# Optimization experiments

Hardware: AMD Instinct MI355X
Metric: run time of the kernel (lower is better)

Reference implementation:

```python
import jax, jax.numpy as jnp
import numpy as np

H = 512  # hidden_size

def setup_inputs() -> dict:
    key = jax.random.key(0)
    ks = jax.random.split(key, 5)
    B, S = 2, 512
    feats = jax.random.normal(ks[0], (B, S, H), dtype=jnp.float32)
    # torch Linear init ~ U(-1/sqrt(in), 1/sqrt(in)); scaled normals are fine for a reference
    W1 = jax.random.normal(ks[1], (2 * H, H), dtype=jnp.float32) / np.sqrt(2 * H)
    b1 = jnp.zeros((H,), dtype=jnp.float32)
    W2 = jax.random.normal(ks[2], (H, H // 2), dtype=jnp.float32) / np.sqrt(H)
    b2 = jnp.zeros((H // 2,), dtype=jnp.float32)
    W3 = jax.random.normal(ks[3], (H // 2, 1), dtype=jnp.float32) / np.sqrt(H // 2)
    b3 = jnp.zeros((1,), dtype=jnp.float32)
    return {"features": feats, "W1": W1, "b1": b1, "W2": W2, "b2": b2, "W3": W3, "b3": b3}


def reference(features, W1, b1, W2, b2, W3, b3):
    # cat([f_i, f_j]) @ W1 == f_i @ W1[:H] + f_j @ W1[H:]
    # Precompute the two halves once per residue instead of per pair.
    a = jnp.einsum('bsh,hk->bsk', features, W1[:H])          # [B,S,H]
    c = jnp.einsum('bsh,hk->bsk', features, W1[H:])          # [B,S,H]
    h1 = jax.nn.relu(a[:, :, None, :] + c[:, None, :, :] + b1)  # [B,S,S,H]
    # Dropout(0.1) is identity at inference.
    h2 = jax.nn.relu(jnp.einsum('bijh,hk->bijk', h1, W2) + b2)  # [B,S,S,H//2]
    logits = jnp.einsum('bijk,ko->bijo', h2, W3) + b3            # [B,S,S,1]
    return jax.nn.sigmoid(logits[..., 0])                        # [B,S,S]
```

## Files before the change

### kernel.cpp

```cpp
#include <hip/hip_runtime.h>

#define S_DIM 512
#define H_DIM 512
#define NH 256
#define TI 8
#define TJ 8

#define AS1 __attribute__((address_space(1)))
#define AS3 __attribute__((address_space(3)))

typedef _Float16 half8 __attribute__((ext_vector_type(8)));
typedef _Float16 half4 __attribute__((ext_vector_type(4)));
typedef float f32x4 __attribute__((ext_vector_type(4)));

__device__ __forceinline__ int swz(int r) { return ((r & 1) << 2) | (r >> 1); }

__global__ __launch_bounds__(256) void convert_all_kernel(const float* __restrict__ feats,
        const float* __restrict__ W1, const float* __restrict__ W2,
        _Float16* __restrict__ f16, _Float16* __restrict__ w1L, _Float16* __restrict__ w2L) {
    int blk = blockIdx.x;
    if (blk < 512) {
        int t = blk * 256 + threadIdx.x;
        float4 v = ((const float4*)feats)[t];
        half4 h;
        h.x = (_Float16)v.x; h.y = (_Float16)v.y; h.z = (_Float16)v.z; h.w = (_Float16)v.w;
        ((half4*)f16)[t] = h;
    } else if (blk < 768) {
        int t = (blk - 512) * 256 + threadIdx.x;
        int gcb = t >> 10, n = t & 1023;
        const float* src = (n < H_DIM) ? &W1[(size_t)(gcb * 8) * H_DIM + n]
                                       : &W1[(size_t)(H_DIM + gcb * 8) * H_DIM + (n - H_DIM)];
        half8 v;
#pragma unroll
        for (int j = 0; j < 8; j++) v[j] = (_Float16)src[(size_t)j * H_DIM];
        *(half8*)&w1L[((size_t)gcb * 1024 + n) * 8] = v;
    } else {
        int t = (blk - 768) * 256 + threadIdx.x;
        int gcb = t >> 8, n = t & 255;
        half8 v;
#pragma unroll
        for (int j = 0; j < 8; j++) v[j] = (_Float16)W2[(size_t)(gcb * 8 + j) * NH + n];
        *(half8*)&w2L[((size_t)gcb * 256 + n) * 8] = v;
    }
}

__global__ __launch_bounds__(256) void prep_mfma_kernel(const _Float16* __restrict__ f16,
        const _Float16* __restrict__ w1L, const float* __restrict__ b1,
        _Float16* __restrict__ aH, _Float16* __restrict__ cH) {
    const int n0 = blockIdx.x * 64, m0 = blockIdx.y * 64;
    const int tid = threadIdx.x, wave = tid >> 6, lane = tid & 63;
    const int quad = lane >> 4, l16 = lane & 15;
    const int wm = wave >> 1, wn = wave & 1;
    int mrow[2], ncol[2];
#pragma unroll
    for (int mt = 0; mt < 2; mt++) mrow[mt] = m0 + wm * 32 + mt * 16 + l16;
#pragma unroll
    for (int nt = 0; nt < 2; nt++) ncol[nt] = n0 + wn * 32 + nt * 16 + l16;
    f32x4 acc[2][2];
#pragma unroll
    for (int mt = 0; mt < 2; mt++)
#pragma unroll
        for (int nt = 0; nt < 2; nt++) acc[mt][nt] = (f32x4)0.f;
#pragma unroll
    for (int ks = 0; ks < 16; ks++) {
        int gcb = ks * 4 + quad;
        half8 af[2], bf[2];
#pragma unroll
        for (int mt = 0; mt < 2; mt++)
            af[mt] = *(const half8*)&f16[(size_t)mrow[mt] * H_DIM + gcb * 8];
#pragma unroll
        for (int nt = 0; nt < 2; nt++)
            bf[nt] = *(const half8*)&w1L[((size_t)gcb * 1024 + ncol[nt]) * 8];
#pragma unroll
        for (int nt = 0; nt < 2; nt++)
#pragma unroll
            for (int mt = 0; mt < 2; mt++)
                acc[mt][nt] = __builtin_amdgcn_mfma_f32_16x16x32_f16(af[mt], bf[nt],
                                                                     acc[mt][nt], 0, 0, 0);
    }
    const bool first_half = (n0 < H_DIM);
#pragma unroll
    for (int nt = 0; nt < 2; nt++) {
        float bias = first_half ? b1[ncol[nt]] : 0.f;
#pragma unroll
        for (int mt = 0; mt < 2; mt++)
#pragma unroll
            for (int r = 0; r < 4; r++) {
                int m = m0 + wm * 32 + mt * 16 + quad * 4 + r;
                float v = acc[mt][nt][r] + bias;
                if (first_half) aH[(size_t)m * H_DIM + ncol[nt]] = (_Float16)v;
                else            cH[(size_t)m * H_DIM + (ncol[nt] - H_DIM)] = (_Float16)v;
            }
    }
}

__global__ __launch_bounds__(256, 4) void pair_kernel(
        const _Float16* __restrict__ aH, const _Float16* __restrict__ cH,
        const _Float16* __restrict__ w2L,
        const float* __restrict__ b2, const float* __restrict__ W3,
        const float* __restrict__ b3, float* __restrict__ out) {
    const int jt = blockIdx.x, it = blockIdx.y, b = blockIdx.z;
    const int i0 = it * TI, j0 = jt * TJ;

    __shared__ __align__(16) _Float16 sa[TI * H_DIM];
    __shared__ __align__(16) _Float16 sc[TJ * H_DIM];
    __shared__ __align__(16) _Float16 afb[2][4][512];
    __shared__ float spart[4][64];

    const int tid = threadIdx.x;
    const int wave = tid >> 6, lane = tid & 63;
    const int quad = lane >> 4, l16 = lane & 15;
    const int nb = wave * 64;

#pragma unroll
    for (int rr0 = 0; rr0 < 2; rr0++) {
        int rr = rr0 * 4 + wave;
        int gc = lane ^ swz(rr & 7);
        __builtin_amdgcn_global_load_lds(
            (const AS1 unsigned int*)&aH[((size_t)(b * S_DIM + i0 + rr)) * H_DIM + gc * 8],
            (AS3 unsigned int*)&sa[rr * H_DIM], 16, 0, 0);
        __builtin_amdgcn_global_load_lds(
            (const AS1 unsigned int*)&cH[((size_t)(b * S_DIM + j0 + rr)) * H_DIM + gc * 8],
            (AS3 unsigned int*)&sc[rr * H_DIM], 16, 0, 0);
    }

    const int hl = l16 >> 3;
    const int ilW = wave * 2 + hl;
    const int saoffW = ilW * H_DIM;
    const int swzAW = swz(ilW);
    const int jl = l16 & 7;
    const int scoff = jl * H_DIM, swzC = swz(jl);

    f32x4 acc[4][4];
#pragma unroll
    for (int mt = 0; mt < 4; mt++)
#pragma unroll
        for (int nt = 0; nt < 4; nt++) acc[mt][nt] = (f32x4)0.f;

    const _Float16* bp = &w2L[((size_t)quad * 256 + nb + l16) * 8];

    half8 bnxt[4];
#pragma unroll
    for (int nt = 0; nt < 4; nt++) bnxt[nt] = *(const half8*)&bp[nt * 16 * 8];

    __syncthreads();

    {
        const int gcb = quad;
        half8 va = *(const half8*)&sa[saoffW + ((gcb ^ swzAW) * 8)];
        half8 vc = *(const half8*)&sc[scoff + ((gcb ^ swzC) * 8)];
        half8 af = __builtin_elementwise_max(va + vc, (half8)(_Float16)0.f);
        *(half8*)&afb[0][wave][lane * 8] = af;
    }
    asm volatile("s_waitcnt lgkmcnt(0)" ::: "memory");
    __builtin_amdgcn_s_barrier();
    __builtin_amdgcn_sched_barrier(0);

#pragma unroll
    for (int ks = 0; ks < 16; ks++) {
        const int buf = ks & 1;
        half8 bf[4];
#pragma unroll
        for (int nt = 0; nt < 4; nt++) bf[nt] = bnxt[nt];
        if (ks < 15) {
            const _Float16* bn = bp + (size_t)4 * 256 * 8;
#pragma unroll
            for (int nt = 0; nt < 4; nt++) bnxt[nt] = *(const half8*)&bn[nt * 16 * 8];
            bp = bn;
            const int gcb = (ks + 1) * 4 + quad;
            half8 va = *(const half8*)&sa[saoffW + ((gcb ^ swzAW) * 8)];
            half8 vc = *(const half8*)&sc[scoff + ((gcb ^ swzC) * 8)];
            half8 af = __builtin_elementwise_max(va + vc, (half8)(_Float16)0.f);
            *(half8*)&afb[buf ^ 1][wave][lane * 8] = af;
        }
        half8 afr[4];
#pragma unroll
        for (int mt = 0; mt < 4; mt++)
            afr[mt] = *(const half8*)&afb[buf][mt][lane * 8];
#pragma unroll
        for (int nt = 0; nt < 4; nt++)
#pragma unroll
            for (int mt = 0; mt < 4; mt++)
                acc[mt][nt] = __builtin_amdgcn_mfma_f32_16x16x32_f16(afr[mt], bf[nt],
                                                                     acc[mt][nt], 0, 0, 0);
        if (ks < 15) {
            asm volatile("s_waitcnt lgkmcnt(0)" ::: "memory");
            __builtin_amdgcn_s_barrier();
            __builtin_amdgcn_sched_barrier(0);
        }
    }

    float b2v[4], w3v[4];
#pragma unroll
    for (int nt = 0; nt < 4; nt++) {
        int n = nb + nt * 16 + l16;
        b2v[nt] = b2[n];
        w3v[nt] = W3[n];
    }
    float ps[4][4];
#pragma unroll
    for (int mt = 0; mt < 4; mt++)
#pragma unroll
        for (int r = 0; r < 4; r++) {
            float s = 0.f;
#pragma unroll
            for (int nt = 0; nt < 4; nt++) {
                float v = acc[mt][nt][r] + b2v[nt];
                v = v > 0.f ? v : 0.f;
                s += v * w3v[nt];
            }
            ps[mt][r] = s;
        }
#pragma unroll
    for (int mt = 0; mt < 4; mt++)
#pragma unroll
        for (int r = 0; r < 4; r++) {
            float s = ps[mt][r];
            s += __shfl_xor(s, 8, 16);
            s += __shfl_xor(s, 4, 16);
            s += __shfl_xor(s, 2, 16);
            s += __shfl_xor(s, 1, 16);
            ps[mt][r] = s;
        }
    if (l16 == 0) {
#pragma unroll
        for (int mt = 0; mt < 4; mt++)
#pragma unroll
            for (int r = 0; r < 4; r++)
                spart[wave][mt * 16 + quad * 4 + r] = ps[mt][r];
    }
    __syncthreads();
    if (tid < 64) {
        float tot = spart[0][tid] + spart[1][tid] + spart[2][tid] + spart[3][tid] + b3[0];
        float sg = 1.f / (1.f + __expf(-tot));
        int i = i0 + (tid >> 3), j = j0 + (tid & 7);
        out[(size_t)b * S_DIM * S_DIM + (size_t)i * S_DIM + j] = sg;
    }
}

extern "C" void kernel_launch(void* const* d_in, const int* in_sizes, int n_in,
                              void* d_out, int out_size, void* d_ws, size_t ws_size,
                              hipStream_t stream) {
    const float* feats = (const float*)d_in[0];
    const float* W1 = (const float*)d_in[1];
    const float* b1 = (const float*)d_in[2];
    const float* W2 = (const float*)d_in[3];
    const float* b2 = (const float*)d_in[4];
    const float* W3 = (const float*)d_in[5];
    const float* b3 = (const float*)d_in[6];
    float* out = (float*)d_out;

    const int B = in_sizes[0] / (S_DIM * H_DIM);
    const int M = B * S_DIM;

    char* ws = (char*)d_ws;
    _Float16* f16  = (_Float16*)ws;
    _Float16* aH   = (_Float16*)(ws + (1 << 20));
    _Float16* cH   = (_Float16*)(ws + (2 << 20));
    _Float16* w1L  = (_Float16*)(ws + (3 << 20));
    _Float16* w2L  = (_Float16*)(ws + (4 << 20));

    convert_all_kernel<<<832, 256, 0, stream>>>(feats, W1, W2, f16, w1L, w2L);
    prep_mfma_kernel<<<dim3(16, M / 64), 256, 0, stream>>>(f16, w1L, b1, aH, cH);
    pair_kernel<<<dim3(S_DIM / TJ, S_DIM / TI, B), 256, 0, stream>>>(aH, cH, w2L, b2, W3, b3, out);
}
```

Before: 201.2 us.

## Switch pair GEMM from 16x16x32 to 32x32x16 MFMA tiles

Replaces the 16x16x32 f16 MFMA tiling (4x4 accumulators per wave) with 32x32x16 MFMAs (2x2 f32x16 accumulators). This changes how the relu(a+c) fragments and the W2 fragments are distributed across lanes and waves, and rewrites the epilogue reduction to match the 32-lane output layout. It also raises wave priority around the MFMA block with s_setprio. The aim is fewer MFMA issues and better operand reuse per instruction, at the cost of a more intricate lane and row mapping that has to stay consistent with the precomputed weight layout.

```diff
diff --git a/kernel.cpp b/kernel.cpp
--- a/kernel.cpp
+++ b/kernel.cpp
@@ -12,6 +12,7 @@
 typedef _Float16 half8 __attribute__((ext_vector_type(8)));
 typedef _Float16 half4 __attribute__((ext_vector_type(4)));
 typedef float f32x4 __attribute__((ext_vector_type(4)));
+typedef float f32x16 __attribute__((ext_vector_type(16)));
 
 __device__ __forceinline__ int swz(int r) { return ((r & 1) << 2) | (r >> 1); }
 
@@ -109,7 +110,7 @@
 
     const int tid = threadIdx.x;
     const int wave = tid >> 6, lane = tid & 63;
-    const int quad = lane >> 4, l16 = lane & 15;
+    const int l32 = lane & 31, hi = lane >> 5;
     const int nb = wave * 64;
 
 #pragma unroll
@@ -124,31 +125,32 @@
             (AS3 unsigned int*)&sc[rr * H_DIM], 16, 0, 0);
     }
 
-    const int hl = l16 >> 3;
-    const int ilW = wave * 2 + hl;
+    const int kstW = wave >> 1, mtW = wave & 1;
+    const int ilW = mtW * 4 + (l32 >> 3);
     const int saoffW = ilW * H_DIM;
     const int swzAW = swz(ilW);
-    const int jl = l16 & 7;
+    const int jl = l32 & 7;
     const int scoff = jl * H_DIM, swzC = swz(jl);
 
-    f32x4 acc[4][4];
-#pragma unroll
-    for (int mt = 0; mt < 4; mt++)
-#pragma unroll
-        for (int nt = 0; nt < 4; nt++) acc[mt][nt] = (f32x4)0.f;
-
-    const _Float16* bp = &w2L[((size_t)quad * 256 + nb + l16) * 8];
+    f32x16 acc[2][2];
+#pragma unroll
+    for (int mt = 0; mt < 2; mt++)
+#pragma unroll
+        for (int nt = 0; nt < 2; nt++) acc[mt][nt] = (f32x16)0.f;
+
+    const _Float16* bp = &w2L[((size_t)(hi * 256 + nb + l32)) * 8];
 
     half8 bnxt[4];
 #pragma unroll
-    for (int nt = 0; nt < 4; nt++) bnxt[nt] = *(const half8*)&bp[nt * 16 * 8];
+    for (int q = 0; q < 4; q++)
+        bnxt[q] = *(const half8*)&bp[(q >> 1) * 4096 + (q & 1) * 256];
 
     __syncthreads();
 
     {
-        const int gcb = quad;
-        half8 va = *(const half8*)&sa[saoffW + ((gcb ^ swzAW) * 8)];
-        half8 vc = *(const half8*)&sc[scoff + ((gcb ^ swzC) * 8)];
+        const int chunk = kstW * 2 + hi;
+        half8 va = *(const half8*)&sa[saoffW + ((chunk ^ swzAW) * 8)];
+        half8 vc = *(const half8*)&sc[scoff + ((chunk ^ swzC) * 8)];
         half8 af = __builtin_elementwise_max(va + vc, (half8)(_Float16)0.f);
         *(half8*)&afb[0][wave][lane * 8] = af;
     }
@@ -161,28 +163,33 @@
         const int buf = ks & 1;
         half8 bf[4];
 #pragma unroll
-        for (int nt = 0; nt < 4; nt++) bf[nt] = bnxt[nt];
+        for (int q = 0; q < 4; q++) bf[q] = bnxt[q];
         if (ks < 15) {
-            const _Float16* bn = bp + (size_t)4 * 256 * 8;
-#pragma unroll
-            for (int nt = 0; nt < 4; nt++) bnxt[nt] = *(const half8*)&bn[nt * 16 * 8];
+            const _Float16* bn = bp + (size_t)8192;
+#pragma unroll
+            for (int q = 0; q < 4; q++)
+                bnxt[q] = *(const half8*)&bn[(q >> 1) * 4096 + (q & 1) * 256];
             bp = bn;
-            const int gcb = (ks + 1) * 4 + quad;
-            half8 va = *(const half8*)&sa[saoffW + ((gcb ^ swzAW) * 8)];
-            half8 vc = *(const half8*)&sc[scoff + ((gcb ^ swzC) * 8)];
+            const int chunk = (ks + 1) * 4 + kstW * 2 + hi;
+            half8 va = *(const half8*)&sa[saoffW + ((chunk ^ swzAW) * 8)];
+            half8 vc = *(const half8*)&sc[scoff + ((chunk ^ swzC) * 8)];
             half8 af = __builtin_elementwise_max(va + vc, (half8)(_Float16)0.f);
             *(half8*)&afb[buf ^ 1][wave][lane * 8] = af;
         }
         half8 afr[4];
 #pragma unroll
-        for (int mt = 0; mt < 4; mt++)
-            afr[mt] = *(const half8*)&afb[buf][mt][lane * 8];
-#pragma unroll
-        for (int nt = 0; nt < 4; nt++)
-#pragma unroll
-            for (int mt = 0; mt < 4; mt++)
-                acc[mt][nt] = __builtin_amdgcn_mfma_f32_16x16x32_f16(afr[mt], bf[nt],
-                                                                     acc[mt][nt], 0, 0, 0);
+        for (int f = 0; f < 4; f++)
+            afr[f] = *(const half8*)&afb[buf][f][lane * 8];
+        __builtin_amdgcn_s_setprio(1);
+#pragma unroll
+        for (int kst = 0; kst < 2; kst++)
+#pragma unroll
+            for (int nt = 0; nt < 2; nt++)
+#pragma unroll
+                for (int mt = 0; mt < 2; mt++)
+                    acc[mt][nt] = __builtin_amdgcn_mfma_f32_32x32x16_f16(
+                            afr[kst * 2 + mt], bf[kst * 2 + nt], acc[mt][nt], 0, 0, 0);
+        __builtin_amdgcn_s_setprio(0);
         if (ks < 15) {
             asm volatile("s_waitcnt lgkmcnt(0)" ::: "memory");
             __builtin_amdgcn_s_barrier();
@@ -190,44 +197,39 @@
         }
     }
 
-    float b2v[4], w3v[4];
-#pragma unroll
-    for (int nt = 0; nt < 4; nt++) {
-        int n = nb + nt * 16 + l16;
+    float b2v[2], w3v[2];
+#pragma unroll
+    for (int nt = 0; nt < 2; nt++) {
+        int n = nb + nt * 32 + l32;
         b2v[nt] = b2[n];
         w3v[nt] = W3[n];
     }
-    float ps[4][4];
-#pragma unroll
-    for (int mt = 0; mt < 4; mt++)
-#pragma unroll
-        for (int r = 0; r < 4; r++) {
+#pragma unroll
+    for (int mt = 0; mt < 2; mt++) {
+        float ps[16];
+#pragma unroll
+        for (int r = 0; r < 16; r++) {
             float s = 0.f;
 #pragma unroll
-            for (int nt = 0; nt < 4; nt++) {
+            for (int nt = 0; nt < 2; nt++) {
                 float v = acc[mt][nt][r] + b2v[nt];
                 v = v > 0.f ? v : 0.f;
                 s += v * w3v[nt];
             }
-            ps[mt][r] = s;
-        }
-#pragma unroll
-    for (int mt = 0; mt < 4; mt++)
-#pragma unroll
-        for (int r = 0; r < 4; r++) {
-            float s = ps[mt][r];
-            s += __shfl_xor(s, 8, 16);
-            s += __shfl_xor(s, 4, 16);
-            s += __shfl_xor(s, 2, 16);
-            s += __shfl_xor(s, 1, 16);
-            ps[mt][r] = s;
-        }
-    if (l16 == 0) {
-#pragma unroll
-        for (int mt = 0; mt < 4; mt++)
-#pragma unroll
-            for (int r = 0; r < 4; r++)
-                spart[wave][mt * 16 + quad * 4 + r] = ps[mt][r];
+            s += __shfl_xor(s, 16, 32);
+            s += __shfl_xor(s, 8, 32);
+            s += __shfl_xor(s, 4, 32);
+            s += __shfl_xor(s, 2, 32);
+            s += __shfl_xor(s, 1, 32);
+            ps[r] = s;
+        }
+        if (l32 == 0) {
+#pragma unroll
+            for (int r = 0; r < 16; r++) {
+                int row = (r & 3) + 8 * (r >> 2) + 4 * hi;
+                spart[wave][mt * 32 + row] = ps[r];
+            }
+        }
     }
     __syncthreads();
     if (tid < 64) {
```

New measurement: 238.4 us. 18.5% more time.
